# Kernel tuning notes

Hardware: AMD Instinct MI355X
Metric: run time of the kernel (lower is better)

## Reference

```python
import jax, jax.numpy as jnp
import numpy as np

IMG_DIM = 512
BATCH = 32


def setup_inputs() -> dict:
    key = jax.random.key(0)
    k1, k2, k3, k4, k5 = jax.random.split(key, 5)
    N, D = BATCH, IMG_DIM
    return {
        "im1": jax.random.normal(k1, (N, 3, D, D), jnp.float32),
        "im2": jax.random.normal(k2, (N, 3, D, D), jnp.float32),
        "C": jax.random.normal(k3, (N, 2, D, D), jnp.float32),
        "M1": jax.random.uniform(k4, (N, 1, D, D), jnp.float32),
        "M2": jax.random.uniform(k5, (N, 1, D, D), jnp.float32),
    }


def _grid_q(D):
    # q[0] = row coord repeated, q[1] = col coord tiled -> [2, D*D]
    x = jnp.arange(D, dtype=jnp.float32)
    return jnp.stack([jnp.repeat(x, D), jnp.tile(x, D)], axis=0)


def _get_pixel(qi, nb_x, nb_y, imflat, D):
    # qi: [N,2,HW]; nb_x, nb_y: [N,HW] integer-valued floats; imflat: [N,3,HW]
    w = (1.0 - jnp.abs(qi[:, 0] - nb_x)) * (1.0 - jnp.abs(qi[:, 1] - nb_y))  # [N,HW]
    inds = (nb_y + D * nb_x).astype(jnp.int32)  # ind = y + D*x, detached from grads
    inds = jax.lax.stop_gradient(inds)
    px = jnp.take_along_axis(imflat, inds[:, None, :], axis=2)  # [N,3,HW]
    return w[:, None, :] * px


def _masked_rp(image, mask, qi_orig, D):
    N = image.shape[0]
    HW = D * D
    imflat = image.reshape(N, 3, HW)
    qi = jnp.clip(qi_orig, 0.001, D - 1.001)  # [N,2,HW]
    fx, fy = jnp.floor(qi[:, 0]), jnp.floor(qi[:, 1])
    cx, cy = jnp.ceil(qi[:, 0]), jnp.ceil(qi[:, 1])
    res = (_get_pixel(qi, fx, fy, imflat, D)
           + _get_pixel(qi, cx, fy, imflat, D)
           + _get_pixel(qi, fx, cy, imflat, D)
           + _get_pixel(qi, cx, cy, imflat, D))  # [N,3,HW]
    oob_loss = jnp.mean((qi_orig - qi) ** 2) / (D * D) * 0.01
    res_img = res.reshape(image.shape)
    return res_img * mask, oob_loss


def _forward(im1, im2, C, M1, M2):
    N = im1.shape[0]
    D = im1.shape[2]
    q = _grid_q(D)[None]  # [1,2,HW]
    Cflat = C.reshape(N, 2, D * D)
    a, la = _masked_rp(im1, M1, q + Cflat, D)
    b, lb = _masked_rp(im2, M2, q - Cflat, D)
    return a + b, la + lb


def reference(im1, im2, C, M1, M2):
    return _forward(im1, im2, C, M1, M2)
```

## Files before the change

### kernel.cpp

```cpp
#include <hip/hip_runtime.h>


constexpr int D    = 512;
constexpr int HW   = D * D;
constexpr int NB   = 32;
constexpr int NPIX = NB * HW;
constexpr float LOSS_SCALE = (float)(0.01 / (2.0 * (double)NPIX * (double)HW));

__device__ __forceinline__ float3 sample_img(const float* __restrict__ im,
                                             float q0o, float q1o, float& oob)
{
    const float hi = (float)(512.0 - 1.001);
    float q0 = fminf(fmaxf(q0o, 0.001f), hi);
    float q1 = fminf(fmaxf(q1o, 0.001f), hi);
    float d0 = q0o - q0, d1 = q1o - q1;
    oob += d0 * d0 + d1 * d1;

    float fx = floorf(q0), fy = floorf(q1);
    float cx = ceilf(q0),  cy = ceilf(q1);
    float wfx = 1.0f - (q0 - fx), wcx = 1.0f - (cx - q0);
    float wfy = 1.0f - (q1 - fy), wcy = 1.0f - (cy - q1);

    int ix0 = (int)fx, iy0 = (int)fy, ix1 = (int)cx, iy1 = (int)cy;
    int iff = iy0 + D * ix0;
    int icf = iy0 + D * ix1;
    int ifc = iy1 + D * ix0;
    int icc = iy1 + D * ix1;

    float wff = wfx * wfy, wcf = wcx * wfy, wfc = wfx * wcy, wcc = wcx * wcy;

    float3 r;
    r.x = wff * im[iff]          + wcf * im[icf]          + wfc * im[ifc]          + wcc * im[icc];
    r.y = wff * im[HW + iff]     + wcf * im[HW + icf]     + wfc * im[HW + ifc]     + wcc * im[HW + icc];
    r.z = wff * im[2 * HW + iff] + wcf * im[2 * HW + icf] + wfc * im[2 * HW + ifc] + wcc * im[2 * HW + icc];
    return r;
}

__global__ void __launch_bounds__(256)
vm_fwd(const float* __restrict__ im1, const float* __restrict__ im2,
       const float* __restrict__ C,   const float* __restrict__ M1,
       const float* __restrict__ M2,  float* __restrict__ out)
{
    float oob = 0.0f;
    int stride = gridDim.x * blockDim.x;
    for (int idx = blockIdx.x * blockDim.x + threadIdx.x; idx < NPIX; idx += stride) {
        int n  = idx >> 18;
        int hw = idx & (HW - 1);
        float qx = (float)(hw >> 9);
        float qy = (float)(hw & (D - 1));

        const float* Cn = C + (size_t)n * 2 * HW;
        float c0 = Cn[hw];
        float c1 = Cn[HW + hw];
        float m1 = M1[idx];
        float m2 = M2[idx];

        const float* p1 = im1 + (size_t)n * 3 * HW;
        const float* p2 = im2 + (size_t)n * 3 * HW;

        float3 a = sample_img(p1, qx + c0, qy + c1, oob);
        float3 b = sample_img(p2, qx - c0, qy - c1, oob);

        size_t obase = (size_t)n * 3 * HW + hw;
        out[obase]          = a.x * m1 + b.x * m2;
        out[obase + HW]     = a.y * m1 + b.y * m2;
        out[obase + 2 * HW] = a.z * m1 + b.z * m2;
    }

    #pragma unroll
    for (int off = 32; off > 0; off >>= 1)
        oob += __shfl_down(oob, off, 64);

    __shared__ float wave_sums[4];
    int lane = threadIdx.x & 63;
    int wave = threadIdx.x >> 6;
    if (lane == 0) wave_sums[wave] = oob;
    __syncthreads();
    if (threadIdx.x == 0) {
        float s = wave_sums[0] + wave_sums[1] + wave_sums[2] + wave_sums[3];
        atomicAdd(out + (size_t)3 * NPIX, s * LOSS_SCALE);
    }
}

extern "C" void kernel_launch(void* const* d_in, const int* in_sizes, int n_in,
                              void* d_out, int out_size, void* d_ws, size_t ws_size,
                              hipStream_t stream) {
    const float* im1 = (const float*)d_in[0];
    const float* im2 = (const float*)d_in[1];
    const float* C   = (const float*)d_in[2];
    const float* M1  = (const float*)d_in[3];
    const float* M2  = (const float*)d_in[4];
    float* out = (float*)d_out;

    hipMemsetAsync(out + (size_t)3 * NPIX, 0, sizeof(float), stream);

    vm_fwd<<<8192, 256, 0, stream>>>(im1, im2, C, M1, M2, out);
}
```

Baseline: 417.6 us.

## Vectorize per-thread 4-pixel processing and simplify bilinear sampling to lerps

Replaces the grid-stride loop with a fixed mapping where each thread handles four consecutive pixels, loading C and masks with float4 loads and writing outputs with float4 nontemporal stores. The bilinear sampling is rewritten as lerps from a single base offset. A scale factor of 2 per axis is applied when the fractional part is zero, reproducing the reference's double-counting when floor equals ceil. This aims to cut load/store instruction count and index arithmetic. It relies on the grid exactly covering all pixels and on the different floating-point ordering being acceptable.

```diff
diff --git a/kernel.cpp b/kernel.cpp
--- a/kernel.cpp
+++ b/kernel.cpp
@@ -7,33 +7,39 @@
 constexpr int NPIX = NB * HW;
 constexpr float LOSS_SCALE = (float)(0.01 / (2.0 * (double)NPIX * (double)HW));
 
-__device__ __forceinline__ float3 sample_img(const float* __restrict__ im,
-                                             float q0o, float q1o, float& oob)
+typedef float f4 __attribute__((ext_vector_type(4)));
+
+__device__ __forceinline__ float3 sample3(const float* __restrict__ p,
+                                          float q0o, float q1o,
+                                          float& oob, float& wscale)
 {
-    const float hi = (float)(512.0 - 1.001);
+    const float hi = 510.999f;
     float q0 = fminf(fmaxf(q0o, 0.001f), hi);
     float q1 = fminf(fmaxf(q1o, 0.001f), hi);
     float d0 = q0o - q0, d1 = q1o - q1;
-    oob += d0 * d0 + d1 * d1;
+    oob = fmaf(d0, d0, oob);
+    oob = fmaf(d1, d1, oob);
 
     float fx = floorf(q0), fy = floorf(q1);
-    float cx = ceilf(q0),  cy = ceilf(q1);
-    float wfx = 1.0f - (q0 - fx), wcx = 1.0f - (cx - q0);
-    float wfy = 1.0f - (q1 - fy), wcy = 1.0f - (cy - q1);
+    float ax = q0 - fx,    ay = q1 - fy;
+    float sc = ((ax == 0.0f) ? 2.0f : 1.0f) * ((ay == 0.0f) ? 2.0f : 1.0f);
+    wscale = sc;
 
-    int ix0 = (int)fx, iy0 = (int)fy, ix1 = (int)cx, iy1 = (int)cy;
-    int iff = iy0 + D * ix0;
-    int icf = iy0 + D * ix1;
-    int ifc = iy1 + D * ix0;
-    int icc = iy1 + D * ix1;
+    int off = (int)fy + (((int)fx) << 9);
 
-    float wff = wfx * wfy, wcf = wcx * wfy, wfc = wfx * wcy, wcc = wcx * wcy;
-
-    float3 r;
-    r.x = wff * im[iff]          + wcf * im[icf]          + wfc * im[ifc]          + wcc * im[icc];
-    r.y = wff * im[HW + iff]     + wcf * im[HW + icf]     + wfc * im[HW + ifc]     + wcc * im[HW + icc];
-    r.z = wff * im[2 * HW + iff] + wcf * im[2 * HW + icf] + wfc * im[2 * HW + ifc] + wcc * im[2 * HW + icc];
-    return r;
+    float r[3];
+    #pragma unroll
+    for (int c = 0; c < 3; ++c) {
+        const float* pc = p + c * HW;
+        float v00 = pc[off];
+        float v01 = pc[off + 1];
+        float v10 = pc[off + 512];
+        float v11 = pc[off + 513];
+        float top = fmaf(ay, v01 - v00, v00);
+        float bot = fmaf(ay, v11 - v10, v10);
+        r[c] = fmaf(ax, bot - top, top);
+    }
+    return make_float3(r[0], r[1], r[2]);
 }
 
 __global__ void __launch_bounds__(256)
@@ -41,31 +47,48 @@
        const float* __restrict__ C,   const float* __restrict__ M1,
        const float* __restrict__ M2,  float* __restrict__ out)
 {
+    const int b  = blockIdx.x;
+    const int n  = b >> 8;
+    const int hw = ((b & 255) << 10) | (threadIdx.x << 2);
+
+    const float qx  = (float)(hw >> 9);
+    const float qy0 = (float)(hw & 511);
+
+    const float* Cn = C   + (size_t)n * 2 * HW;
+    const float* Mp = M1  + (size_t)n * HW;
+    const float* Mq = M2  + (size_t)n * HW;
+    const float* p1 = im1 + (size_t)n * 3 * HW;
+    const float* p2 = im2 + (size_t)n * 3 * HW;
+
+    f4 c0 = *(const f4*)(Cn + hw);
+    f4 c1 = *(const f4*)(Cn + HW + hw);
+    f4 m1 = *(const f4*)(Mp + hw);
+    f4 m2 = *(const f4*)(Mq + hw);
+
     float oob = 0.0f;
-    int stride = gridDim.x * blockDim.x;
-    for (int idx = blockIdx.x * blockDim.x + threadIdx.x; idx < NPIX; idx += stride) {
-        int n  = idx >> 18;
-        int hw = idx & (HW - 1);
-        float qx = (float)(hw >> 9);
-        float qy = (float)(hw & (D - 1));
+    float o0a[4], o1a[4], o2a[4];
 
-        const float* Cn = C + (size_t)n * 2 * HW;
-        float c0 = Cn[hw];
-        float c1 = Cn[HW + hw];
-        float m1 = M1[idx];
-        float m2 = M2[idx];
+    #pragma unroll
+    for (int j = 0; j < 4; ++j) {
+        float qyj = qy0 + (float)j;
+        float sA, sB;
+        float3 av = sample3(p1, qx + c0[j], qyj + c1[j], oob, sA);
+        float3 bv = sample3(p2, qx - c0[j], qyj - c1[j], oob, sB);
+        float w1 = m1[j] * sA;
+        float w2 = m2[j] * sB;
+        o0a[j] = fmaf(av.x, w1, bv.x * w2);
+        o1a[j] = fmaf(av.y, w1, bv.y * w2);
+        o2a[j] = fmaf(av.z, w1, bv.z * w2);
+    }
 
-        const float* p1 = im1 + (size_t)n * 3 * HW;
-        const float* p2 = im2 + (size_t)n * 3 * HW;
+    f4 o0 = {o0a[0], o0a[1], o0a[2], o0a[3]};
+    f4 o1 = {o1a[0], o1a[1], o1a[2], o1a[3]};
+    f4 o2 = {o2a[0], o2a[1], o2a[2], o2a[3]};
 
-        float3 a = sample_img(p1, qx + c0, qy + c1, oob);
-        float3 b = sample_img(p2, qx - c0, qy - c1, oob);
-
-        size_t obase = (size_t)n * 3 * HW + hw;
-        out[obase]          = a.x * m1 + b.x * m2;
-        out[obase + HW]     = a.y * m1 + b.y * m2;
-        out[obase + 2 * HW] = a.z * m1 + b.z * m2;
-    }
+    size_t obase = (size_t)n * 3 * HW + hw;
+    __builtin_nontemporal_store(o0, (f4*)(out + obase));
+    __builtin_nontemporal_store(o1, (f4*)(out + obase + HW));
+    __builtin_nontemporal_store(o2, (f4*)(out + obase + 2 * HW));
 
     #pragma unroll
     for (int off = 32; off > 0; off >>= 1)
```

Result: faster. 408.8 us (-2.1%).
